# Kernel tuning notes

Measured on AMD Instinct MI355X. Metric: run time of the kernel, lower is better.

Reference implementation:

```python
import jax, jax.numpy as jnp
import numpy as np

B, C, O, N, T, K = 4, 64, 64, 32768, 4, 9
PAD, DIL = 4, 1  # padding*dilation, dilation
SIGMA = 0.05
EPS_BN = 1e-5


def _gather_ch(x, idx):
    # x: [B, C, N], idx: [B, N] -> gather along last dim per channel
    idx3 = jnp.broadcast_to(idx[:, None, :], x.shape)
    return jnp.take_along_axis(x, idx3, axis=-1)


def _weighted_conv(x, coords, w):
    # x: [B,C,N], coords: [B,3,N], w: [O,C,K]
    xp = jnp.pad(x, ((0, 0), (0, 0), (PAD, PAD)))
    cp = jnp.pad(coords, ((0, 0), (0, 0), (PAD, PAD)))
    win_idx = jnp.arange(N)[:, None] + jnp.arange(K) * DIL  # [N, K]
    win = xp[:, :, win_idx]   # [B,C,N,K]
    cwin = cp[:, :, win_idx]  # [B,3,N,K]
    d = cwin - cwin[:, :, :, K // 2:K // 2 + 1]
    s = jnp.sum(d * d, axis=1)                    # [B,N,K]
    r = jnp.sqrt(jnp.where(s > 0, s, 1.0))
    r = jnp.where(s > 0, r, 0.0)
    wgt = jnp.maximum(1.0 - r / SIGMA, 0.0)       # [B,N,K]
    return jnp.einsum('bcnk,bnk,ock->bon', win, wgt, w)


def _bn(x, g, b):
    # training-mode BatchNorm1d over (B, N)
    m = jnp.mean(x, axis=(0, 2), keepdims=True)
    v = jnp.var(x, axis=(0, 2), keepdims=True)
    return g[None, :, None] * (x - m) * jax.lax.rsqrt(v + EPS_BN) + b[None, :, None]


def setup_inputs() -> dict:
    key = jax.random.key(0)
    ks = jax.random.split(key, 12)
    inp = jax.random.normal(ks[0], (B, C, N), dtype=jnp.float32)
    # coords in a small box so sigma=0.05 yields non-trivial weights
    multi_coords = jax.random.uniform(ks[1], (B, 3, N, T), dtype=jnp.float32) * 0.02
    indices = jax.random.randint(ks[2], (B, N, T), 0, N, dtype=jnp.int32)
    reindices = jax.random.randint(ks[3], (B, N, T), 0, N, dtype=jnp.int32)
    fan = C * K
    conv_w = jax.random.normal(ks[4], (T, O, C, K), dtype=jnp.float32) / np.sqrt(fan)
    bn_gamma = jnp.ones((T, O), dtype=jnp.float32)
    bn_beta = jnp.zeros((T, O), dtype=jnp.float32)
    fusion_w = jax.random.normal(ks[5], (O, T * O), dtype=jnp.float32) / np.sqrt(T * O)
    fusion_b = jnp.zeros((O,), dtype=jnp.float32)
    fusion_gamma = jnp.ones((O,), dtype=jnp.float32)
    fusion_beta = jnp.zeros((O,), dtype=jnp.float32)
    return {"input": inp, "multi_coords": multi_coords, "indices": indices,
            "reindices": reindices, "conv_w": conv_w, "bn_gamma": bn_gamma,
            "bn_beta": bn_beta, "fusion_w": fusion_w, "fusion_b": fusion_b,
            "fusion_gamma": fusion_gamma, "fusion_beta": fusion_beta}


def reference(input, multi_coords, indices, reindices, conv_w, bn_gamma, bn_beta,
              fusion_w, fusion_b, fusion_gamma, fusion_beta):
    outs = []
    for i in range(T):  # fixed small set of 4 Hilbert orders
        x = _gather_ch(input, indices[:, :, i])            # [B,C,N]
        x = _weighted_conv(x, multi_coords[:, :, :, i], conv_w[i])  # [B,O,N]
        x = _bn(x, bn_gamma[i], bn_beta[i])
        x = _gather_ch(x, reindices[:, :, i])
        outs.append(x)
    cat = jnp.concatenate(outs, axis=1)                    # [B, T*O, N]
    y = jnp.einsum('bcn,oc->bon', cat, fusion_w) + fusion_b[None, :, None]
    y = _bn(y, fusion_gamma, fusion_beta)
    return jax.nn.relu(y)
```

## Files before the change

### kernel.cpp

```cpp
#include <hip/hip_runtime.h>
#include <hip/hip_bf16.h>

#define BB 4
#define CC 64
#define OO 64
#define NN 32768
#define TT 4
#define KK 9
#define PADW 4
#define SIGMA 0.05f
#define EPS_BN 1e-5f

typedef __attribute__((ext_vector_type(8))) short bf16x8;
typedef __attribute__((ext_vector_type(4))) float f32x4;

__device__ __forceinline__ unsigned short f2bf(float f) {
  __hip_bfloat16 h = __float2bfloat16(f);
  return *reinterpret_cast<unsigned short*>(&h);
}
__device__ __forceinline__ unsigned int pkbf(float a, float b) {
  float2 t; t.x = a; t.y = b;
  __hip_bfloat162 h = __float22bfloat162_rn(t);
  unsigned int r;
  __builtin_memcpy(&r, &h, 4);
  return r;
}

__global__ __launch_bounds__(256) void transpose_kernel(
    const float* __restrict__ inp, unsigned short* __restrict__ xTb)
{
  const int n0 = blockIdx.x * 64;
  const int b  = blockIdx.y;
  const int tid = threadIdx.x;
  __shared__ float xt[64][65];
  {
    int nl = tid & 63, c4 = tid >> 6;
    #pragma unroll
    for (int i = 0; i < 16; ++i) {
      int c = c4 * 16 + i;
      xt[c][nl] = inp[((size_t)(b*CC + c))*NN + n0 + nl];
    }
  }
  __syncthreads();
  {
    int nl = tid >> 2, cq = tid & 3;
    unsigned int pk[8];
    #pragma unroll
    for (int i = 0; i < 8; ++i) {
      int c = cq*16 + i*2;
      pk[i] = pkbf(xt[c][nl], xt[c+1][nl]);
    }
    unsigned int* dst = (unsigned int*)(xTb + (((size_t)b*NN) + n0 + nl)*CC + cq*16);
    ((int4*)dst)[0] = make_int4((int)pk[0],(int)pk[1],(int)pk[2],(int)pk[3]);
    ((int4*)dst)[1] = make_int4((int)pk[4],(int)pk[5],(int)pk[6],(int)pk[7]);
  }
}

__global__ __launch_bounds__(256) void wprep_kernel(
    const float* __restrict__ cw, unsigned short* __restrict__ W4)
{
  const int k = blockIdx.x;
  const int t = blockIdx.y;
  for (int u = threadIdx.x; u < OO*CC; u += 256) {
    int o = u >> 6, c = u & 63;
    int ow = o >> 5, ot = (o >> 4) & 1, l15 = o & 15;
    int frag = c >> 5, q = (c >> 3) & 3, j = c & 7;
    float wv = cw[(((size_t)(t*OO + o))*CC + c)*KK + k];
    W4[(size_t)(t*9+k)*4096 + ow*2048 + ot*1024 + frag*512 + l15*32 + q*8 + j]
        = f2bf(wv);
  }
}

__global__ __launch_bounds__(256, 4) void conv_kernel(
    const unsigned short* __restrict__ xTb,
    const float* __restrict__ mc,
    const int*   __restrict__ ind,
    const unsigned short* __restrict__ W4,
    unsigned short* __restrict__ Y,
    float* __restrict__ cpart2)
{
  const int n0  = blockIdx.x * 128;
  const int b   = blockIdx.y;
  const int t   = blockIdx.z;
  const int tid = threadIdx.x;
  const int lane = tid & 63;
  const int w    = tid >> 6;
  const int l15  = lane & 15;
  const int q    = lane >> 4;
  const int ow   = w & 1;
  const int nw   = w >> 1;

  __shared__ short xg[136][72];
  __shared__ float wgl[128][10];
  __shared__ float mcs[3][140];

  int4 g[5];
  #pragma unroll
  for (int i = 0; i < 5; ++i) {
    int u = tid + 256*i;
    g[i] = make_int4(0,0,0,0);
    if (u < 1088) {
      int p = u >> 3, s = u & 7;
      int m = n0 + p - PADW;
      if (m >= 0 && m < NN) {
        int idx = ind[((size_t)b*NN + m)*TT + t];
        g[i] = *(const int4*)(xTb + ((size_t)b*NN + idx)*CC + s*8);
      }
    }
  }

  if (tid < 136) {
    int m = n0 + tid - PADW;
    #pragma unroll
    for (int d = 0; d < 3; ++d) {
      float4 v = make_float4(0.f, 0.f, 0.f, 0.f);
      if (m >= 0 && m < NN)
        v = *(const float4*)(mc + (((size_t)(b*3+d))*NN + m)*TT);
      mcs[d][tid] = (t==0) ? v.x : (t==1) ? v.y : (t==2) ? v.z : v.w;
    }
  }

  #pragma unroll
  for (int i = 0; i < 5; ++i) {
    int u = tid + 256*i;
    if (u < 1088) {
      int p = u >> 3, s = u & 7;
      *(int4*)&xg[p][s*8] = g[i];
    }
  }
  __syncthreads();

  {
    int nl = tid >> 1;
    int k0 = (tid & 1) * 5;
    int kc = 5 - (tid & 1);
    float cx = mcs[0][nl+4], cy = mcs[1][nl+4], cz = mcs[2][nl+4];
    for (int i2 = 0; i2 < kc; ++i2) {
      int k = k0 + i2, mi = nl + k;
      float dx = mcs[0][mi]-cx, dy = mcs[1][mi]-cy, dz = mcs[2][mi]-cz;
      float s2 = dx*dx + dy*dy + dz*dz;
      float r = (s2 > 0.f) ? sqrtf(s2) : 0.f;
      wgl[nl][k] = fmaxf(1.f - r*(1.f/SIGMA), 0.f);
    }
  }
  __syncthreads();

  const unsigned short* Wt = W4 + (size_t)t*9*4096 + ow*2048 + (l15*4 + q)*8;
  const f32x4 Z = {0.f, 0.f, 0.f, 0.f};
  f32x4 fin[2][4];
  #pragma unroll
  for (int ot = 0; ot < 2; ++ot)
    #pragma unroll
    for (int ns = 0; ns < 4; ++ns) fin[ot][ns] = Z;

  for (int k = 0; k < KK; ++k) {
    const unsigned short* Wk = Wt + (size_t)k*4096;
    bf16x8 af[2][2];
    #pragma unroll
    for (int ot = 0; ot < 2; ++ot) {
      af[ot][0] = *(const bf16x8*)(Wk + ot*1024);
      af[ot][1] = *(const bf16x8*)(Wk + ot*1024 + 512);
    }
    #pragma unroll
    for (int ns = 0; ns < 4; ++ns) {
      int nl = nw*64 + ns*16 + l15;
      int p  = nl + k;
      bf16x8 b0 = *(const bf16x8*)&xg[p][q*8];
      bf16x8 b1 = *(const bf16x8*)&xg[p][32 + q*8];
      float wgt = wgl[nl][k];
      #pragma unroll
      for (int ot = 0; ot < 2; ++ot) {
        f32x4 d = __builtin_amdgcn_mfma_f32_16x16x32_bf16(af[ot][0], b0, Z, 0, 0, 0);
        d = __builtin_amdgcn_mfma_f32_16x16x32_bf16(af[ot][1], b1, d, 0, 0, 0);
        fin[ot][ns] += wgt * d;
      }
    }
  }

  #pragma unroll
  for (int ns = 0; ns < 4; ++ns) {
    int nl = nw*64 + ns*16 + l15;
    size_t row = (((size_t)t*BB + b)*NN + n0 + nl)*OO;
    #pragma unroll
    for (int ot = 0; ot < 2; ++ot) {
      uint2 pk2;
      pk2.x = pkbf(fin[ot][ns][0], fin[ot][ns][1]);
      pk2.y = pkbf(fin[ot][ns][2], fin[ot][ns][3]);
      *(uint2*)(Y + row + ow*32 + ot*16 + q*4) = pk2;
    }
  }

  float sv[16];
  #pragma unroll
  for (int ot = 0; ot < 2; ++ot)
    #pragma unroll
    for (int r = 0; r < 4; ++r) {
      float a = 0.f, qs = 0.f;
      #pragma unroll
      for (int ns = 0; ns < 4; ++ns) {
        float v = fin[ot][ns][r];
        a += v; qs += v*v;
      }
      sv[ot*4+r] = a; sv[8+ot*4+r] = qs;
    }
  #pragma unroll
  for (int msk = 1; msk < 16; msk <<= 1) {
    #pragma unroll
    for (int i = 0; i < 16; ++i) sv[i] += __shfl_xor(sv[i], msk, 16);
  }
  if (l15 == 0) {
    int slot4 = ((b*256 + (int)blockIdx.x) << 2) | w;
    #pragma unroll
    for (int ot = 0; ot < 2; ++ot)
      #pragma unroll
      for (int r = 0; r < 4; ++r) {
        int o = ow*32 + ot*16 + q*4 + r;
        cpart2[((size_t)((t*64 + o)*2 + 0))*4096 + slot4] = sv[ot*4+r];
        cpart2[((size_t)((t*64 + o)*2 + 1))*4096 + slot4] = sv[8+ot*4+r];
      }
  }
}

__global__ __launch_bounds__(256) void bnparam_kernel(
    const float* __restrict__ cpart2,
    const float* __restrict__ gam,
    const float* __restrict__ bet,
    float* __restrict__ ss)
{
  const int to = blockIdx.x;
  const int tid = threadIdx.x;
  __shared__ float r1[256], r2[256];
  const float* p1 = cpart2 + (size_t)to*2*4096;
  const float* p2 = p1 + 4096;
  float s1 = 0.f, s2 = 0.f;
  for (int i = tid*4; i < 4096; i += 1024) {
    float4 a = *(const float4*)(p1 + i);
    float4 c = *(const float4*)(p2 + i);
    s1 += a.x + a.y + a.z + a.w;
    s2 += c.x + c.y + c.z + c.w;
  }
  r1[tid] = s1; r2[tid] = s2;
  __syncthreads();
  for (int st = 128; st > 0; st >>= 1) {
    if (tid < st) { r1[tid] += r1[tid+st]; r2[tid] += r2[tid+st]; }
    __syncthreads();
  }
  if (tid == 0) {
    const float inv = 1.f / (float)(BB * NN);
    float mean = r1[0] * inv;
    float var  = r2[0] * inv - mean * mean;
    float sc = gam[to] * rsqrtf(var + EPS_BN);
    ss[to*2 + 0] = sc;
    ss[to*2 + 1] = bet[to] - mean * sc;
  }
}

__global__ __launch_bounds__(256) void fusion_kernel(
    const unsigned short* __restrict__ Y,
    const int*   __restrict__ rind,
    const float* __restrict__ ss,
    const float* __restrict__ fw,
    const float* __restrict__ fb,
    float* __restrict__ out)
{
  const int n0  = blockIdx.x * 128;
  const int b   = blockIdx.y;
  const int tid = threadIdx.x;
  const int lane = tid & 63;
  const int w    = tid >> 6;
  const int l15  = lane & 15;
  const int q    = lane >> 4;
  const int ow   = w & 1;
  const int nw   = w >> 1;

  __shared__ short zg[128][72];
  __shared__ int   rnl[TT][128];
  __shared__ float scl[256];
  __shared__ float b2l[64];
  __shared__ float bred[4][64];

  if (tid < 128) {
    int4 r4 = *(const int4*)(rind + ((size_t)b*NN + n0 + tid)*TT);
    rnl[0][tid] = r4.x; rnl[1][tid] = r4.y;
    rnl[2][tid] = r4.z; rnl[3][tid] = r4.w;
  }
  scl[tid] = ss[tid*2];
  {
    int o = tid & 63, g = tid >> 6;
    const float* wp = fw + (size_t)o*256 + g*64;
    float s = 0.f;
    for (int j = 0; j < 64; ++j) s += wp[j] * ss[(g*64 + j)*2 + 1];
    bred[g][o] = s;
  }
  __syncthreads();
  if (tid < 64)
    b2l[tid] = fb[tid] + bred[0][tid] + bred[1][tid] + bred[2][tid] + bred[3][tid];

  f32x4 fin[2][4];
  #pragma unroll
  for (int ot = 0; ot < 2; ++ot)
    #pragma unroll
    for (int ns = 0; ns < 4; ++ns) fin[ot][ns] = (f32x4){0.f,0.f,0.f,0.f};

  for (int r = 0; r < 4; ++r) {
    if (r) __syncthreads();
    const unsigned short* Yb = Y + ((size_t)r*BB + b)*NN*OO;
    #pragma unroll
    for (int i = 0; i < 4; ++i) {
      int u = tid + 256*i;
      int n = u >> 3, s = u & 7;
      int rn = rnl[r][n];
      *(int4*)&zg[n][s*8] = *(const int4*)(Yb + (size_t)rn*OO + s*8);
    }
    __syncthreads();

    #pragma unroll
    for (int kk = 0; kk < 2; ++kk) {
      bf16x8 af[2];
      #pragma unroll
      for (int ot = 0; ot < 2; ++ot) {
        const float* wp = fw + (size_t)(ow*32 + ot*16 + l15)*256 + r*64 + kk*32 + q*8;
        const float* sp = scl + r*64 + kk*32 + q*8;
        unsigned int pk[4];
        #pragma unroll
        for (int j = 0; j < 4; ++j)
          pk[j] = pkbf(wp[2*j]*sp[2*j], wp[2*j+1]*sp[2*j+1]);
        int4 tmp = make_int4((int)pk[0],(int)pk[1],(int)pk[2],(int)pk[3]);
        __builtin_memcpy(&af[ot], &tmp, 16);
      }
      #pragma unroll
      for (int ns = 0; ns < 4; ++ns) {
        int nl = nw*64 + ns*16 + l15;
        bf16x8 bfr = *(const bf16x8*)&zg[nl][kk*32 + q*8];
        #pragma unroll
        for (int ot = 0; ot < 2; ++ot)
          fin[ot][ns] = __builtin_amdgcn_mfma_f32_16x16x32_bf16(af[ot], bfr, fin[ot][ns], 0, 0, 0);
      }
    }
  }

  #pragma unroll
  for (int ot = 0; ot < 2; ++ot)
    #pragma unroll
    for (int rr = 0; rr < 4; ++rr) {
      int o = ow*32 + ot*16 + q*4 + rr;
      float bias = b2l[o];
      float* dst = out + ((size_t)(b*OO + o))*NN + n0 + nw*64;
      #pragma unroll
      for (int ns = 0; ns < 4; ++ns)
        dst[ns*16 + l15] = fin[ot][ns][rr] + bias;
    }
}

__global__ __launch_bounds__(256) void fstat_kernel(
    const float* __restrict__ out, float* __restrict__ fpart)
{
  const int o = blockIdx.x, b = blockIdx.y;
  const int tid = threadIdx.x;
  __shared__ float r1[256], r2[256];
  const float* src = out + ((size_t)(b*OO + o))*NN;
  float s1 = 0.f, s2 = 0.f;
  for (int i = tid*4; i < NN; i += 1024) {
    float4 v = *(const float4*)(src + i);
    s1 += v.x + v.y + v.z + v.w;
    s2 += v.x*v.x + v.y*v.y + v.z*v.z + v.w*v.w;
  }
  r1[tid] = s1; r2[tid] = s2;
  __syncthreads();
  for (int st = 128; st > 0; st >>= 1) {
    if (tid < st) { r1[tid] += r1[tid+st]; r2[tid] += r2[tid+st]; }
    __syncthreads();
  }
  if (tid == 0) {
    fpart[(b*OO + o)*2 + 0] = r1[0];
    fpart[(b*OO + o)*2 + 1] = r2[0];
  }
}

__global__ __launch_bounds__(256) void final_kernel(
    float* __restrict__ out, const float* __restrict__ fpart,
    const float* __restrict__ fg, const float* __restrict__ fbeta)
{
  __shared__ float fssl[128];
  const int tid = threadIdx.x;
  if (tid < 64) {
    float s1 = 0.f, s2 = 0.f;
    #pragma unroll
    for (int b = 0; b < BB; ++b) {
      s1 += fpart[(b*OO + tid)*2 + 0];
      s2 += fpart[(b*OO + tid)*2 + 1];
    }
    const float inv = 1.f / (float)(BB * NN);
    float mean = s1 * inv;
    float var  = s2 * inv - mean * mean;
    float sc = fg[tid] * rsqrtf(var + EPS_BN);
    fssl[tid*2 + 0] = sc;
    fssl[tid*2 + 1] = fbeta[tid] - mean * sc;
  }
  __syncthreads();
  const size_t base = (size_t)blockIdx.x * 2048 + tid * 4;
  #pragma unroll
  for (int s = 0; s < 2; ++s) {
    size_t e = base + (size_t)s * 1024;
    int o2 = (int)((e >> 15) & 63);
    float sc = fssl[o2*2 + 0];
    float sh = fssl[o2*2 + 1];
    float4 v = *(float4*)(out + e);
    v.x = fmaxf(v.x*sc + sh, 0.f);
    v.y = fmaxf(v.y*sc + sh, 0.f);
    v.z = fmaxf(v.z*sc + sh, 0.f);
    v.w = fmaxf(v.w*sc + sh, 0.f);
    *(float4*)(out + e) = v;
  }
}

extern "C" void kernel_launch(void* const* d_in, const int* in_sizes, int n_in,
                              void* d_out, int out_size, void* d_ws, size_t ws_size,
                              hipStream_t stream) {
  const float* inp  = (const float*)d_in[0];
  const float* mc   = (const float*)d_in[1];
  const int*   ind  = (const int*)  d_in[2];
  const int*   rind = (const int*)  d_in[3];
  const float* cw   = (const float*)d_in[4];
  const float* bg   = (const float*)d_in[5];
  const float* bb   = (const float*)d_in[6];
  const float* fw   = (const float*)d_in[7];
  const float* fb   = (const float*)d_in[8];
  const float* fg   = (const float*)d_in[9];
  const float* fbt  = (const float*)d_in[10];

  char* ws = (char*)d_ws;
  float* convss = (float*)(ws + 0);
  float* fpart  = (float*)(ws + 2560);
  unsigned short* Y = (unsigned short*)(ws + 8192);

  char* ob = (char*)d_out;
  unsigned short* xTb = (unsigned short*)ob;
  unsigned short* W4  = (unsigned short*)(ob + 16777216);
  float*          cpart2 = (float*)(ob + 17072128);
  float* out = (float*)d_out;

  dim3 gt(NN/64, BB);
  transpose_kernel<<<gt, 256, 0, stream>>>(inp, xTb);

  dim3 gw(KK, TT);
  wprep_kernel<<<gw, 256, 0, stream>>>(cw, W4);

  dim3 gc(NN/128, BB, TT);
  conv_kernel<<<gc, 256, 0, stream>>>(xTb, mc, ind, W4, Y, cpart2);

  bnparam_kernel<<<256, 256, 0, stream>>>(cpart2, bg, bb, convss);

  dim3 gf(NN/128, BB);
  fusion_kernel<<<gf, 256, 0, stream>>>(Y, rind, convss, fw, fb, out);

  dim3 gs(OO, BB);
  fstat_kernel<<<gs, 256, 0, stream>>>(out, fpart);

  final_kernel<<<(BB*OO*NN)/2048, 256, 0, stream>>>(out, fpart, fg, fbt);
}
```

Before: 242.8 us.

## Loop over orders inside conv kernel with prefetch of next gather; merge prep kernels

The conv kernel now handles all four Hilbert orders in one block instead of one order per block. The coordinates and indices for all orders are loaded once into shared memory. The gather and weight computation for the next order are issued into registers while the current order's MFMA loop runs, which hides gather latency. The transpose and weight-prep kernels are merged into one launch. In exchange the grid has four times fewer blocks, each block runs longer with more register pressure, and the extra syncs add serialization.

```diff
diff --git a/kernel.cpp b/kernel.cpp
--- a/kernel.cpp
+++ b/kernel.cpp
@@ -26,48 +26,49 @@
   return r;
 }
 
-__global__ __launch_bounds__(256) void transpose_kernel(
-    const float* __restrict__ inp, unsigned short* __restrict__ xTb)
+__global__ __launch_bounds__(256) void prep_kernel(
+    const float* __restrict__ inp, unsigned short* __restrict__ xTb,
+    const float* __restrict__ cw,  unsigned short* __restrict__ W4)
 {
-  const int n0 = blockIdx.x * 64;
-  const int b  = blockIdx.y;
+  const int bx = blockIdx.x;
   const int tid = threadIdx.x;
   __shared__ float xt[64][65];
-  {
-    int nl = tid & 63, c4 = tid >> 6;
-    #pragma unroll
-    for (int i = 0; i < 16; ++i) {
-      int c = c4 * 16 + i;
-      xt[c][nl] = inp[((size_t)(b*CC + c))*NN + n0 + nl];
-    }
-  }
-  __syncthreads();
-  {
-    int nl = tid >> 2, cq = tid & 3;
-    unsigned int pk[8];
-    #pragma unroll
-    for (int i = 0; i < 8; ++i) {
-      int c = cq*16 + i*2;
-      pk[i] = pkbf(xt[c][nl], xt[c+1][nl]);
-    }
-    unsigned int* dst = (unsigned int*)(xTb + (((size_t)b*NN) + n0 + nl)*CC + cq*16);
-    ((int4*)dst)[0] = make_int4((int)pk[0],(int)pk[1],(int)pk[2],(int)pk[3]);
-    ((int4*)dst)[1] = make_int4((int)pk[4],(int)pk[5],(int)pk[6],(int)pk[7]);
-  }
-}
-
-__global__ __launch_bounds__(256) void wprep_kernel(
-    const float* __restrict__ cw, unsigned short* __restrict__ W4)
-{
-  const int k = blockIdx.x;
-  const int t = blockIdx.y;
-  for (int u = threadIdx.x; u < OO*CC; u += 256) {
-    int o = u >> 6, c = u & 63;
-    int ow = o >> 5, ot = (o >> 4) & 1, l15 = o & 15;
-    int frag = c >> 5, q = (c >> 3) & 3, j = c & 7;
-    float wv = cw[(((size_t)(t*OO + o))*CC + c)*KK + k];
-    W4[(size_t)(t*9+k)*4096 + ow*2048 + ot*1024 + frag*512 + l15*32 + q*8 + j]
-        = f2bf(wv);
+
+  if (bx < 2048) {
+    const int n0 = (bx & 511) * 64;
+    const int b  = bx >> 9;
+    {
+      int nl = tid & 63, c4 = tid >> 6;
+      #pragma unroll
+      for (int i = 0; i < 16; ++i) {
+        int c = c4 * 16 + i;
+        xt[c][nl] = inp[((size_t)(b*CC + c))*NN + n0 + nl];
+      }
+    }
+    __syncthreads();
+    {
+      int nl = tid >> 2, cq = tid & 3;
+      unsigned int pk[8];
+      #pragma unroll
+      for (int i = 0; i < 8; ++i) {
+        int c = cq*16 + i*2;
+        pk[i] = pkbf(xt[c][nl], xt[c+1][nl]);
+      }
+      unsigned int* dst = (unsigned int*)(xTb + (((size_t)b*NN) + n0 + nl)*CC + cq*16);
+      ((int4*)dst)[0] = make_int4((int)pk[0],(int)pk[1],(int)pk[2],(int)pk[3]);
+      ((int4*)dst)[1] = make_int4((int)pk[4],(int)pk[5],(int)pk[6],(int)pk[7]);
+    }
+  } else {
+    const int u0 = bx - 2048;
+    const int k = u0 % 9, t = u0 / 9;
+    for (int u = tid; u < OO*CC; u += 256) {
+      int o = u >> 6, c = u & 63;
+      int ow = o >> 5, ot = (o >> 4) & 1, l15 = o & 15;
+      int frag = c >> 5, q = (c >> 3) & 3, j = c & 7;
+      float wv = cw[(((size_t)(t*OO + o))*CC + c)*KK + k];
+      W4[(size_t)(t*9+k)*4096 + ow*2048 + ot*1024 + frag*512 + l15*32 + q*8 + j]
+          = f2bf(wv);
+    }
   }
 }
 
@@ -81,7 +82,6 @@
 {
   const int n0  = blockIdx.x * 128;
   const int b   = blockIdx.y;
-  const int t   = blockIdx.z;
   const int tid = threadIdx.x;
   const int lane = tid & 63;
   const int w    = tid >> 6;
@@ -90,11 +90,32 @@
   const int ow   = w & 1;
   const int nw   = w >> 1;
 
-  __shared__ short xg[136][72];
-  __shared__ float wgl[128][10];
-  __shared__ float mcs[3][140];
-
-  int4 g[5];
+  __shared__ short  xg[136][72];
+  __shared__ float  wgl[128][10];
+  __shared__ float4 mcs4[3][140];
+  __shared__ int    idxs[136][4];
+
+  if (tid < 136) {
+    int m = n0 + tid - PADW;
+    bool v = (m >= 0 && m < NN);
+    #pragma unroll
+    for (int d = 0; d < 3; ++d) {
+      float4 c4 = make_float4(0.f,0.f,0.f,0.f);
+      if (v) c4 = *(const float4*)(mc + (((size_t)(b*3+d))*NN + m)*TT);
+      mcs4[d][tid] = c4;
+    }
+    int4 i4 = make_int4(0,0,0,0);
+    if (v) i4 = *(const int4*)(ind + ((size_t)b*NN + m)*TT);
+    *(int4*)&idxs[tid][0] = i4;
+  }
+  __syncthreads();
+
+  const int nlh = tid >> 1;
+  const int k0  = (tid & 1) * 5;
+
+  int4  g[5];
+  float wr[5];
+
   #pragma unroll
   for (int i = 0; i < 5; ++i) {
     int u = tid + 256*i;
@@ -103,121 +124,153 @@
       int p = u >> 3, s = u & 7;
       int m = n0 + p - PADW;
       if (m >= 0 && m < NN) {
-        int idx = ind[((size_t)b*NN + m)*TT + t];
+        int idx = idxs[p][0];
         g[i] = *(const int4*)(xTb + ((size_t)b*NN + idx)*CC + s*8);
       }
     }
   }
-
-  if (tid < 136) {
-    int m = n0 + tid - PADW;
-    #pragma unroll
-    for (int d = 0; d < 3; ++d) {
-      float4 v = make_float4(0.f, 0.f, 0.f, 0.f);
-      if (m >= 0 && m < NN)
-        v = *(const float4*)(mc + (((size_t)(b*3+d))*NN + m)*TT);
-      mcs[d][tid] = (t==0) ? v.x : (t==1) ? v.y : (t==2) ? v.z : v.w;
-    }
-  }
-
+  {
+    float cx = ((const float*)&mcs4[0][nlh+4])[0];
+    float cy = ((const float*)&mcs4[1][nlh+4])[0];
+    float cz = ((const float*)&mcs4[2][nlh+4])[0];
+    #pragma unroll
+    for (int i = 0; i < 5; ++i) {
+      int mi = nlh + k0 + i;
+      float dx = ((const float*)&mcs4[0][mi])[0] - cx;
+      float dy = ((const float*)&mcs4[1][mi])[0] - cy;
+      float dz = ((const float*)&mcs4[2][mi])[0] - cz;
+      float s2 = dx*dx + dy*dy + dz*dz;
+      float r = (s2 > 0.f) ? sqrtf(s2) : 0.f;
+      wr[i] = fmaxf(1.f - r*(1.f/SIGMA), 0.f);
+    }
+  }
   #pragma unroll
   for (int i = 0; i < 5; ++i) {
     int u = tid + 256*i;
-    if (u < 1088) {
-      int p = u >> 3, s = u & 7;
-      *(int4*)&xg[p][s*8] = g[i];
-    }
-  }
+    if (u < 1088) { int p = u >> 3, s = u & 7; *(int4*)&xg[p][s*8] = g[i]; }
+  }
+  #pragma unroll
+  for (int i = 0; i < 5; ++i) wgl[nlh][k0+i] = wr[i];
   __syncthreads();
 
-  {
-    int nl = tid >> 1;
-    int k0 = (tid & 1) * 5;
-    int kc = 5 - (tid & 1);
-    float cx = mcs[0][nl+4], cy = mcs[1][nl+4], cz = mcs[2][nl+4];
-    for (int i2 = 0; i2 < kc; ++i2) {
-      int k = k0 + i2, mi = nl + k;
-      float dx = mcs[0][mi]-cx, dy = mcs[1][mi]-cy, dz = mcs[2][mi]-cz;
-      float s2 = dx*dx + dy*dy + dz*dz;
-      float r = (s2 > 0.f) ? sqrtf(s2) : 0.f;
-      wgl[nl][k] = fmaxf(1.f - r*(1.f/SIGMA), 0.f);
-    }
-  }
-  __syncthreads();
-
-  const unsigned short* Wt = W4 + (size_t)t*9*4096 + ow*2048 + (l15*4 + q)*8;
   const f32x4 Z = {0.f, 0.f, 0.f, 0.f};
-  f32x4 fin[2][4];
-  #pragma unroll
-  for (int ot = 0; ot < 2; ++ot)
-    #pragma unroll
-    for (int ns = 0; ns < 4; ++ns) fin[ot][ns] = Z;
-
-  for (int k = 0; k < KK; ++k) {
-    const unsigned short* Wk = Wt + (size_t)k*4096;
-    bf16x8 af[2][2];
-    #pragma unroll
-    for (int ot = 0; ot < 2; ++ot) {
-      af[ot][0] = *(const bf16x8*)(Wk + ot*1024);
-      af[ot][1] = *(const bf16x8*)(Wk + ot*1024 + 512);
-    }
+
+  for (int t = 0; t < TT; ++t) {
+    if (t < 3) {
+      int tn = t + 1;
+      #pragma unroll
+      for (int i = 0; i < 5; ++i) {
+        int u = tid + 256*i;
+        g[i] = make_int4(0,0,0,0);
+        if (u < 1088) {
+          int p = u >> 3, s = u & 7;
+          int m = n0 + p - PADW;
+          if (m >= 0 && m < NN) {
+            int idx = idxs[p][tn];
+            g[i] = *(const int4*)(xTb + ((size_t)b*NN + idx)*CC + s*8);
+          }
+        }
+      }
+      float cx = ((const float*)&mcs4[0][nlh+4])[tn];
+      float cy = ((const float*)&mcs4[1][nlh+4])[tn];
+      float cz = ((const float*)&mcs4[2][nlh+4])[tn];
+      #pragma unroll
+      for (int i = 0; i < 5; ++i) {
+        int mi = nlh + k0 + i;
+        float dx = ((const float*)&mcs4[0][mi])[tn] - cx;
+        float dy = ((const float*)&mcs4[1][mi])[tn] - cy;
+        float dz = ((const float*)&mcs4[2][mi])[tn] - cz;
+        float s2 = dx*dx + dy*dy + dz*dz;
+        float r = (s2 > 0.f) ? sqrtf(s2) : 0.f;
+        wr[i] = fmaxf(1.f - r*(1.f/SIGMA), 0.f);
+      }
+    }
+
+    const unsigned short* Wt = W4 + (size_t)t*9*4096 + ow*2048 + (l15*4 + q)*8;
+    f32x4 fin[2][4];
+    #pragma unroll
+    for (int ot = 0; ot < 2; ++ot)
+      #pragma unroll
+      for (int ns = 0; ns < 4; ++ns) fin[ot][ns] = Z;
+
+    for (int k = 0; k < KK; ++k) {
+      const unsigned short* Wk = Wt + (size_t)k*4096;
+      bf16x8 af[2][2];
+      #pragma unroll
+      for (int ot = 0; ot < 2; ++ot) {
+        af[ot][0] = *(const bf16x8*)(Wk + ot*1024);
+        af[ot][1] = *(const bf16x8*)(Wk + ot*1024 + 512);
+      }
+      #pragma unroll
+      for (int ns = 0; ns < 4; ++ns) {
+        int nl = nw*64 + ns*16 + l15;
+        int p  = nl + k;
+        bf16x8 b0 = *(const bf16x8*)&xg[p][q*8];
+        bf16x8 b1 = *(const bf16x8*)&xg[p][32 + q*8];
+        float wgt = wgl[nl][k];
+        #pragma unroll
+        for (int ot = 0; ot < 2; ++ot) {
+          f32x4 d = __builtin_amdgcn_mfma_f32_16x16x32_bf16(af[ot][0], b0, Z, 0, 0, 0);
+          d = __builtin_amdgcn_mfma_f32_16x16x32_bf16(af[ot][1], b1, d, 0, 0, 0);
+          fin[ot][ns] += wgt * d;
+        }
+      }
+    }
+
     #pragma unroll
     for (int ns = 0; ns < 4; ++ns) {
       int nl = nw*64 + ns*16 + l15;
-      int p  = nl + k;
-      bf16x8 b0 = *(const bf16x8*)&xg[p][q*8];
-      bf16x8 b1 = *(const bf16x8*)&xg[p][32 + q*8];
-      float wgt = wgl[nl][k];
+      size_t row = (((size_t)t*BB + b)*NN + n0 + nl)*OO;
       #pragma unroll
       for (int ot = 0; ot < 2; ++ot) {
-        f32x4 d = __builtin_amdgcn_mfma_f32_16x16x32_bf16(af[ot][0], b0, Z, 0, 0, 0);
-        d = __builtin_amdgcn_mfma_f32_16x16x32_bf16(af[ot][1], b1, d, 0, 0, 0);
-        fin[ot][ns] += wgt * d;
-      }
-    }
-  }
-
-  #pragma unroll
-  for (int ns = 0; ns < 4; ++ns) {
-    int nl = nw*64 + ns*16 + l15;
-    size_t row = (((size_t)t*BB + b)*NN + n0 + nl)*OO;
-    #pragma unroll
-    for (int ot = 0; ot < 2; ++ot) {
-      uint2 pk2;
-      pk2.x = pkbf(fin[ot][ns][0], fin[ot][ns][1]);
-      pk2.y = pkbf(fin[ot][ns][2], fin[ot][ns][3]);
-      *(uint2*)(Y + row + ow*32 + ot*16 + q*4) = pk2;
-    }
-  }
-
-  float sv[16];
-  #pragma unroll
-  for (int ot = 0; ot < 2; ++ot)
-    #pragma unroll
-    for (int r = 0; r < 4; ++r) {
-      float a = 0.f, qs = 0.f;
-      #pragma unroll
-      for (int ns = 0; ns < 4; ++ns) {
-        float v = fin[ot][ns][r];
-        a += v; qs += v*v;
-      }
-      sv[ot*4+r] = a; sv[8+ot*4+r] = qs;
-    }
-  #pragma unroll
-  for (int msk = 1; msk < 16; msk <<= 1) {
-    #pragma unroll
-    for (int i = 0; i < 16; ++i) sv[i] += __shfl_xor(sv[i], msk, 16);
-  }
-  if (l15 == 0) {
-    int slot4 = ((b*256 + (int)blockIdx.x) << 2) | w;
+        uint2 pk2;
+        pk2.x = pkbf(fin[ot][ns][0], fin[ot][ns][1]);
+        pk2.y = pkbf(fin[ot][ns][2], fin[ot][ns][3]);
+        *(uint2*)(Y + row + ow*32 + ot*16 + q*4) = pk2;
+      }
+    }
+
+    float sv[16];
     #pragma unroll
     for (int ot = 0; ot < 2; ++ot)
       #pragma unroll
       for (int r = 0; r < 4; ++r) {
-        int o = ow*32 + ot*16 + q*4 + r;
-        cpart2[((size_t)((t*64 + o)*2 + 0))*4096 + slot4] = sv[ot*4+r];
-        cpart2[((size_t)((t*64 + o)*2 + 1))*4096 + slot4] = sv[8+ot*4+r];
-      }
+        float a = 0.f, qs = 0.f;
+        #pragma unroll
+        for (int ns = 0; ns < 4; ++ns) {
+          float v = fin[ot][ns][r];
+          a += v; qs += v*v;
+        }
+        sv[ot*4+r] = a; sv[8+ot*4+r] = qs;
+      }
+    #pragma unroll
+    for (int msk = 1; msk < 16; msk <<= 1) {
+      #pragma unroll
+      for (int i = 0; i < 16; ++i) sv[i] += __shfl_xor(sv[i], msk, 16);
+    }
+    if (l15 == 0) {
+      int slot4 = ((b*256 + (int)blockIdx.x) << 2) | w;
+      #pragma unroll
+      for (int ot = 0; ot < 2; ++ot)
+        #pragma unroll
+        for (int r = 0; r < 4; ++r) {
+          int o = ow*32 + ot*16 + q*4 + r;
+          cpart2[((size_t)((t*64 + o)*2 + 0))*4096 + slot4] = sv[ot*4+r];
+          cpart2[((size_t)((t*64 + o)*2 + 1))*4096 + slot4] = sv[8+ot*4+r];
+        }
+    }
+
+    if (t < 3) {
+      __syncthreads();
+      #pragma unroll
+      for (int i = 0; i < 5; ++i) {
+        int u = tid + 256*i;
+        if (u < 1088) { int p = u >> 3, s = u & 7; *(int4*)&xg[p][s*8] = g[i]; }
+      }
+      #pragma unroll
+      for (int i = 0; i < 5; ++i) wgl[nlh][k0+i] = wr[i];
+      __syncthreads();
+    }
   }
 }
 
@@ -440,13 +493,9 @@
   float*          cpart2 = (float*)(ob + 17072128);
   float* out = (float*)d_out;
 
-  dim3 gt(NN/64, BB);
-  transpose_kernel<<<gt, 256, 0, stream>>>(inp, xTb);
-
-  dim3 gw(KK, TT);
-  wprep_kernel<<<gw, 256, 0, stream>>>(cw, W4);
-
-  dim3 gc(NN/128, BB, TT);
+  prep_kernel<<<2084, 256, 0, stream>>>(inp, xTb, cw, W4);
+
+  dim3 gc(NN/128, BB);
   conv_kernel<<<gc, 256, 0, stream>>>(xTb, mc, ind, W4, Y, cpart2);
 
   bnparam_kernel<<<256, 256, 0, stream>>>(cpart2, bg, bb, convss);
```

Result: slower. 248.7 us (+2.4%).
